# Optimization experiments

Measured on AMD Instinct MI355X. Metric: run time of the kernel, lower is better.

## Reference

```python
import jax, jax.numpy as jnp
import numpy as np

EMBED = 768
HEAD = 64
SEQ = 4096
BATCH = 4


def setup_inputs() -> dict:
    key = jax.random.key(0)
    ks = jax.random.split(key, 7)
    s = 1.0 / np.sqrt(EMBED)
    x = jax.random.normal(ks[0], (BATCH, SEQ, EMBED), dtype=jnp.float32)
    Wq = jax.random.uniform(ks[1], (EMBED, HEAD), jnp.float32, -s, s)
    bq = jax.random.uniform(ks[2], (HEAD,), jnp.float32, -s, s)
    Wk = jax.random.uniform(ks[3], (EMBED, HEAD), jnp.float32, -s, s)
    bk = jax.random.uniform(ks[4], (HEAD,), jnp.float32, -s, s)
    Wv = jax.random.uniform(ks[5], (EMBED, HEAD), jnp.float32, -s, s)
    bv = jax.random.uniform(ks[6], (HEAD,), jnp.float32, -s, s)
    return {"x": x, "Wq": Wq, "bq": bq, "Wk": Wk, "bk": bk, "Wv": Wv, "bv": bv}


def reference(x, Wq, bq, Wk, bk, Wv, bv):
    # x: [B,T,E]
    Q = x @ Wq + bq  # [B,T,H]
    K = x @ Wk + bk
    V = x @ Wv + bv
    scale = 1.0 / jnp.sqrt(jnp.asarray(HEAD, dtype=x.dtype))
    wei = jnp.einsum('bqh,bkh->bqk', Q, K) * scale  # [B,T,T]
    T = x.shape[1]
    causal = jnp.tril(jnp.ones((T, T), dtype=bool))
    wei = jnp.where(causal, wei, -jnp.inf)
    wei = jax.nn.softmax(wei, axis=-1)
    return jnp.einsum('bqk,bkh->bqh', wei, V)  # [B,T,H]
```

## Files before the change

### kernel.cpp

```cpp
#include <hip/hip_runtime.h>


#define BB 4
#define TT 4096
#define EE 768
#define HH 64
#define BT (BB*TT)

typedef __attribute__((ext_vector_type(8))) short short8;
typedef __attribute__((ext_vector_type(4))) float f32x4;
#define MFMA16(a,b,c) __builtin_amdgcn_mfma_f32_16x16x32_bf16(a,b,c,0,0,0)
#define QSCALE 0.18033688011112042f

static __device__ __forceinline__ float bflo(unsigned a){ return __uint_as_float(a << 16); }
static __device__ __forceinline__ unsigned short f2bf(float f){
    unsigned x = __float_as_uint(f);
    x += 0x7fffu + ((x >> 16) & 1u);
    return (unsigned short)(x >> 16);
}
template<int FP32>
static __device__ __forceinline__ float ldin(const void* p, int idx){
    if (FP32) return ((const float*)p)[idx];
    return bflo(((const unsigned short*)p)[idx]);
}

template<int FP32>
static __device__ void wt_body(const void* W, int wi, int e0, unsigned short* wt){
    __shared__ unsigned short ts[64 * 72];
    const int tid = threadIdx.x;
    #pragma unroll
    for (int p = 0; p < 2; p++){
        int i = p * 256 + tid;
        int r = i >> 3, g = i & 7;
        unsigned short v[8];
        if (FP32){
            const float* src = (const float*)W + (size_t)(e0 + r) * HH + g * 8;
            const float4 a = *(const float4*)src, b = *(const float4*)(src + 4);
            v[0]=f2bf(a.x); v[1]=f2bf(a.y); v[2]=f2bf(a.z); v[3]=f2bf(a.w);
            v[4]=f2bf(b.x); v[5]=f2bf(b.y); v[6]=f2bf(b.z); v[7]=f2bf(b.w);
        } else {
            const unsigned short* src = (const unsigned short*)W + (size_t)(e0 + r) * HH + g * 8;
            #pragma unroll
            for (int j = 0; j < 8; j++) v[j] = src[j];
        }
        #pragma unroll
        for (int j = 0; j < 8; j++) ts[r * 72 + g * 8 + j] = v[j];
    }
    __syncthreads();
    #pragma unroll
    for (int p = 0; p < 2; p++){
        int i = p * 256 + tid;
        int h = i >> 3, g = i & 7;
        unsigned short v[8];
        #pragma unroll
        for (int j = 0; j < 8; j++) v[j] = ts[(g * 8 + j) * 72 + h];
        unsigned short* dst = wt + (size_t)(wi * 64 + h) * EE + e0 + g * 8;
        uint4 pk;
        pk.x = (unsigned)v[0] | ((unsigned)v[1] << 16);
        pk.y = (unsigned)v[2] | ((unsigned)v[3] << 16);
        pk.z = (unsigned)v[4] | ((unsigned)v[5] << 16);
        pk.w = (unsigned)v[6] | ((unsigned)v[7] << 16);
        *(uint4*)dst = pk;
    }
}
__global__ __launch_bounds__(256) void wt_kernel(
    const unsigned short* xu, const void* Wq, const void* Wk, const void* Wv,
    unsigned short* wt, int* flag){
    __shared__ int cnt;
    const int tid = threadIdx.x;
    if (tid == 0) cnt = 0;
    __syncthreads();
    int c = 0;
    #pragma unroll
    for (int i = 0; i < 16; i++){
        unsigned u = xu[tid * 16 + i];
        unsigned e = (u >> 7) & 0xFFu;
        if (e >= 140u) c++;
    }
    atomicAdd(&cnt, c);
    __syncthreads();
    const int fp32 = (cnt > 32) ? 1 : 0;
    if (blockIdx.x == 0 && tid == 0) *flag = fp32;
    const int wi = blockIdx.x / 12;
    const int e0 = (blockIdx.x % 12) * 64;
    const void* W = (wi == 0) ? Wq : (wi == 1) ? Wk : Wv;
    if (fp32) wt_body<1>(W, wi, e0, wt);
    else      wt_body<0>(W, wi, e0, wt);
}

template<int FP32>
static __device__ void qkv_body(const void* x, const unsigned short* wt,
    const void* bq, const void* bk, const void* bv,
    unsigned short* Qw, unsigned short* Kw, unsigned short* VTw,
    unsigned short* xs, unsigned short* wsl)
{
    const int tid = threadIdx.x, lane = tid & 63, w = tid >> 6;
    const int l15 = lane & 15, quad = lane >> 4;
    const int z = blockIdx.x;
    const int m0 = (z >> 1) * 32;
    const int nh = z & 1;
    const int rh = (w & 1) * 16;
    const int ngl = (w >> 1) * 3;

    f32x4 acc[3];
    #pragma unroll
    for (int i = 0; i < 3; i++) acc[i] = (f32x4)(0.f);

    const int srow = tid >> 3, sg = tid & 7;

    for (int c = 0; c < 12; c++){
        const int c0 = c * 64;
        __syncthreads();
        {
            short8 v;
            if (FP32){
                const float* src = (const float*)x + (size_t)(m0 + srow) * EE + c0 + sg * 8;
                const float4 a = *(const float4*)src, b2 = *(const float4*)(src + 4);
                v[0]=(short)f2bf(a.x); v[1]=(short)f2bf(a.y); v[2]=(short)f2bf(a.z); v[3]=(short)f2bf(a.w);
                v[4]=(short)f2bf(b2.x); v[5]=(short)f2bf(b2.y); v[6]=(short)f2bf(b2.z); v[7]=(short)f2bf(b2.w);
            } else {
                v = *(const short8*)((const unsigned short*)x + (size_t)(m0 + srow) * EE + c0 + sg * 8);
            }
            *(short8*)&xs[srow * 72 + sg * 8] = v;
        }
        #pragma unroll
        for (int p = 0; p < 3; p++){
            int i = p * 256 + tid;
            int n = i >> 3, g2 = i & 7;
            *(short8*)&wsl[n * 72 + g2 * 8] =
                *(const short8*)(wt + (size_t)(nh * 96 + n) * EE + c0 + g2 * 8);
        }
        __syncthreads();
        #pragma unroll
        for (int kst = 0; kst < 2; kst++){
            const short8 a = *(const short8*)&xs[(rh + l15) * 72 + kst * 32 + quad * 8];
            #pragma unroll
            for (int nf = 0; nf < 3; nf++){
                const short8 bfr = *(const short8*)&wsl[((ngl + nf) * 16 + l15) * 72 + kst * 32 + quad * 8];
                acc[nf] = MFMA16(a, bfr, acc[nf]);
            }
        }
    }
    #pragma unroll
    for (int nf = 0; nf < 3; nf++){
        const int gi = nh * 6 + ngl + nf;
        const int wi = gi >> 2;
        const int h = (gi & 3) * 16 + l15;
        const void* bp = (wi == 0) ? bq : (wi == 1) ? bk : bv;
        const float bias = ldin<FP32>(bp, h);
        if (wi == 0){
            #pragma unroll
            for (int rr = 0; rr < 4; rr++){
                const int tok = m0 + rh + quad * 4 + rr;
                Qw[(size_t)tok * HH + h] = f2bf((acc[nf][rr] + bias) * QSCALE);
            }
        } else if (wi == 1){
            #pragma unroll
            for (int rr = 0; rr < 4; rr++){
                const int tok = m0 + rh + quad * 4 + rr;
                Kw[(size_t)tok * HH + h] = f2bf(acc[nf][rr] + bias);
            }
        } else {
            const int tok0 = m0 + rh + quad * 4;
            const int bloc = tok0 >> 12;
            const int tl = tok0 & 4095;
            uint2 pk;
            pk.x = (unsigned)f2bf(acc[nf][0] + bias) | ((unsigned)f2bf(acc[nf][1] + bias) << 16);
            pk.y = (unsigned)f2bf(acc[nf][2] + bias) | ((unsigned)f2bf(acc[nf][3] + bias) << 16);
            *(uint2*)&VTw[(size_t)(bloc * 64 + h) * TT + tl] = pk;
        }
    }
}
__global__ __launch_bounds__(256, 4) void qkv_kernel(
    const void* x, const unsigned short* wt,
    const void* bq, const void* bk, const void* bv,
    unsigned short* Qw, unsigned short* Kw, unsigned short* VTw, const int* flag){
    __shared__ unsigned short xs[32 * 72];
    __shared__ unsigned short wsl[96 * 72];
    if (*flag) qkv_body<1>(x, wt, bq, bk, bv, Qw, Kw, VTw, xs, wsl);
    else       qkv_body<0>(x, wt, bq, bk, bv, Qw, Kw, VTw, xs, wsl);
}

__global__ __launch_bounds__(512, 2) void attn_kernel(
    const unsigned short* __restrict__ Q,
    const unsigned short* __restrict__ K, const unsigned short* __restrict__ VT,
    void* __restrict__ out, const int* __restrict__ flag)
{
    __shared__ unsigned short sbuf[8][2304];
    __shared__ float lpart[8][32];

    const int mode = *flag;
    const int z = blockIdx.x;
    const int half = z >> 8;
    const int i0 = z & 255;
    const int b = i0 & 3;
    const int qt = half ? (i0 >> 2) : (127 - (i0 >> 2));
    const int q0 = qt * 32;
    const int nkb = (qt >> 1) + 1;
    const int tid = threadIdx.x;
    const int lane = tid & 63;
    const int w = tid >> 6;
    const int l15 = lane & 15, quad = lane >> 4;
    const int brow = b * TT;

    f32x4 O[2][4];
    float lsum[2][4];
    #pragma unroll
    for (int mt = 0; mt < 2; mt++)
        #pragma unroll
        for (int i = 0; i < 4; i++){ O[mt][i] = (f32x4)(0.f); lsum[mt][i] = 0.f; }

    if (w < nkb){
        short8 qf[2][2];
        #pragma unroll
        for (int mt = 0; mt < 2; mt++)
            #pragma unroll
            for (int kst = 0; kst < 2; kst++)
                qf[mt][kst] = *(const short8*)(Q + (size_t)(brow + q0 + mt * 16 + l15) * HH + kst * 32 + quad * 8);

        short8 kf[4][2];
        #pragma unroll
        for (int c = 0; c < 4; c++)
            #pragma unroll
            for (int kst = 0; kst < 2; kst++)
                kf[c][kst] = *(const short8*)(K + (size_t)(brow + w * 64 + c * 16 + l15) * HH + kst * 32 + quad * 8);

        for (int u = w; u < nkb; u += 8){
            const int k0 = u * 64;
            f32x4 sacc[2][4];
            #pragma unroll
            for (int mt = 0; mt < 2; mt++)
                #pragma unroll
                for (int c = 0; c < 4; c++){
                    sacc[mt][c] = (f32x4)(0.f);
                    sacc[mt][c] = MFMA16(qf[mt][0], kf[c][0], sacc[mt][c]);
                    sacc[mt][c] = MFMA16(qf[mt][1], kf[c][1], sacc[mt][c]);
                }
            short8 vf[4][2];
            #pragma unroll
            for (int c = 0; c < 4; c++)
                #pragma unroll
                for (int kst = 0; kst < 2; kst++)
                    vf[c][kst] = *(const short8*)(VT + (size_t)(b * 64 + c * 16 + l15) * TT + k0 + kst * 32 + quad * 8);
            if (u + 8 < nkb){
                const int kn0 = (u + 8) * 64;
                #pragma unroll
                for (int c = 0; c < 4; c++)
                    #pragma unroll
                    for (int kst = 0; kst < 2; kst++)
                        kf[c][kst] = *(const short8*)(K + (size_t)(brow + kn0 + c * 16 + l15) * HH + kst * 32 + quad * 8);
            }
            const bool diag = (u == nkb - 1);
            #pragma unroll
            for (int mt = 0; mt < 2; mt++){
                #pragma unroll
                for (int c = 0; c < 4; c++){
                    #pragma unroll
                    for (int rr = 0; rr < 4; rr++){
                        float sv = sacc[mt][c][rr];
                        if (diag){
                            const int kg = k0 + c * 16 + l15;
                            const int qg = q0 + mt * 16 + quad * 4 + rr;
                            sv = (kg <= qg) ? sv : -1e30f;
                        }
                        const float p = exp2f(sv);
                        lsum[mt][rr] += p;
                        sbuf[w][mt * 1152 + (quad * 4 + rr) * 72 + c * 16 + l15] = f2bf(p);
                    }
                }
            }
            #pragma unroll
            for (int mt = 0; mt < 2; mt++){
                const short8 pf0 = *(const short8*)&sbuf[w][mt * 1152 + l15 * 72 + quad * 8];
                const short8 pf1 = *(const short8*)&sbuf[w][mt * 1152 + l15 * 72 + 32 + quad * 8];
                #pragma unroll
                for (int c2 = 0; c2 < 4; c2++){
                    O[mt][c2] = MFMA16(pf0, vf[c2][0], O[mt][c2]);
                    O[mt][c2] = MFMA16(pf1, vf[c2][1], O[mt][c2]);
                }
            }
        }
        #pragma unroll
        for (int mt = 0; mt < 2; mt++)
            #pragma unroll
            for (int rr = 0; rr < 4; rr++){
                #pragma unroll
                for (int off = 1; off < 16; off <<= 1)
                    lsum[mt][rr] += __shfl_xor(lsum[mt][rr], off, 64);
            }
    }
    #pragma unroll
    for (int mt = 0; mt < 2; mt++)
        #pragma unroll
        for (int rr = 0; rr < 4; rr++){
            const int row = mt * 16 + quad * 4 + rr;
            #pragma unroll
            for (int c2 = 0; c2 < 4; c2++)
                sbuf[w][row * 72 + c2 * 16 + l15] = f2bf(O[mt][c2][rr]);
            if (l15 == 0) lpart[w][row] = lsum[mt][rr];
        }
    __syncthreads();
    #pragma unroll
    for (int i = 0; i < 4; i++){
        const int e = i * 512 + tid;
        const int r = e >> 6, h = e & 63;
        float num = 0.f, den = 0.f;
        #pragma unroll
        for (int ww = 0; ww < 8; ww++){
            num += bflo(sbuf[ww][r * 72 + h]);
            den += lpart[ww][r];
        }
        const float ov = num / den;
        const size_t gi = (size_t)(brow + q0 + r) * HH + h;
        if (mode) ((float*)out)[gi] = ov;
        else      ((unsigned short*)out)[gi] = f2bf(ov);
    }
}

extern "C" void kernel_launch(void* const* d_in, const int* in_sizes, int n_in,
                              void* d_out, int out_size, void* d_ws, size_t ws_size,
                              hipStream_t stream) {
    const void* x  = d_in[0];
    const void* Wq = d_in[1];
    const void* bq = d_in[2];
    const void* Wk = d_in[3];
    const void* bk = d_in[4];
    const void* Wv = d_in[5];
    const void* bv = d_in[6];

    unsigned short* Qw  = (unsigned short*)d_ws;
    unsigned short* Kw  = Qw + (size_t)BT * HH;
    unsigned short* VTw = Kw + (size_t)BT * HH;
    unsigned short* wt  = VTw + (size_t)BT * HH;
    int* flag  = (int*)(wt + (size_t)192 * EE);

    wt_kernel<<<36, 256, 0, stream>>>((const unsigned short*)x, Wq, Wk, Wv, wt, flag);
    qkv_kernel<<<1024, 256, 0, stream>>>(x, wt, bq, bk, bv, Qw, Kw, VTw, flag);
    attn_kernel<<<512, 512, 0, stream>>>(Qw, Kw, VTw, d_out, flag);
}
```

Before: 167.4 us.

## Split causal attention KV range across two blocks and add combine kernel

Each query tile's key/value range is now split into two halves handled by separate blocks, doubling the attention grid. Each block writes unnormalized partial numerators and denominators to workspace. A new combine kernel sums the two halves, normalizes, and writes the output in fp32 or bf16. This is meant to shorten the critical path of the longest causal tiles and balance work across CUs, at the cost of extra fp32 partial traffic to global memory and one more kernel launch.

```diff
diff --git a/kernel.cpp b/kernel.cpp
--- a/kernel.cpp
+++ b/kernel.cpp
@@ -184,19 +184,22 @@
 __global__ __launch_bounds__(512, 2) void attn_kernel(
     const unsigned short* __restrict__ Q,
     const unsigned short* __restrict__ K, const unsigned short* __restrict__ VT,
-    void* __restrict__ out, const int* __restrict__ flag)
+    float* __restrict__ pnum, float* __restrict__ pden)
 {
     __shared__ unsigned short sbuf[8][2304];
     __shared__ float lpart[8][32];
 
-    const int mode = *flag;
     const int z = blockIdx.x;
-    const int half = z >> 8;
-    const int i0 = z & 255;
+    const int half = z >> 9;
+    const int i0 = z & 511;
     const int b = i0 & 3;
-    const int qt = half ? (i0 >> 2) : (127 - (i0 >> 2));
+    const int qt = 127 - (i0 >> 2);
     const int q0 = qt * 32;
     const int nkb = (qt >> 1) + 1;
+    const int hk = (nkb + 1) >> 1;
+    const int u0 = half ? hk : 0;
+    const int u1 = half ? nkb : hk;
+    const int cnt = u1 - u0;
     const int tid = threadIdx.x;
     const int lane = tid & 63;
     const int w = tid >> 6;
@@ -210,7 +213,7 @@
         #pragma unroll
         for (int i = 0; i < 4; i++){ O[mt][i] = (f32x4)(0.f); lsum[mt][i] = 0.f; }
 
-    if (w < nkb){
+    if (w < cnt){
         short8 qf[2][2];
         #pragma unroll
         for (int mt = 0; mt < 2; mt++)
@@ -223,9 +226,9 @@
         for (int c = 0; c < 4; c++)
             #pragma unroll
             for (int kst = 0; kst < 2; kst++)
-                kf[c][kst] = *(const short8*)(K + (size_t)(brow + w * 64 + c * 16 + l15) * HH + kst * 32 + quad * 8);
-
-        for (int u = w; u < nkb; u += 8){
+                kf[c][kst] = *(const short8*)(K + (size_t)(brow + (u0 + w) * 64 + c * 16 + l15) * HH + kst * 32 + quad * 8);
+
+        for (int u = u0 + w; u < u1; u += 8){
             const int k0 = u * 64;
             f32x4 sacc[2][4];
             #pragma unroll
@@ -242,7 +245,7 @@
                 #pragma unroll
                 for (int kst = 0; kst < 2; kst++)
                     vf[c][kst] = *(const short8*)(VT + (size_t)(b * 64 + c * 16 + l15) * TT + k0 + kst * 32 + quad * 8);
-            if (u + 8 < nkb){
+            if (u + 8 < u1){
                 const int kn0 = (u + 8) * 64;
                 #pragma unroll
                 for (int c = 0; c < 4; c++)
@@ -300,6 +303,7 @@
             if (l15 == 0) lpart[w][row] = lsum[mt][rr];
         }
     __syncthreads();
+    const size_t pbase = ((size_t)half * 512 + i0) * 2048;
     #pragma unroll
     for (int i = 0; i < 4; i++){
         const int e = i * 512 + tid;
@@ -310,10 +314,50 @@
             num += bflo(sbuf[ww][r * 72 + h]);
             den += lpart[ww][r];
         }
-        const float ov = num / den;
-        const size_t gi = (size_t)(brow + q0 + r) * HH + h;
-        if (mode) ((float*)out)[gi] = ov;
-        else      ((unsigned short*)out)[gi] = f2bf(ov);
+        pnum[pbase + e] = num;
+        if (h == 0) pden[((size_t)half * 512 + i0) * 32 + r] = den;
+    }
+}
+
+__global__ __launch_bounds__(256) void combine_kernel(
+    const float* __restrict__ pnum, const float* __restrict__ pden,
+    void* __restrict__ out, const int* __restrict__ flag)
+{
+    const int mode = *flag;
+    const int g = blockIdx.x * 256 + threadIdx.x;
+    const int e0 = g * 8;
+    const int pidx = e0 >> 11;
+    const int o = e0 & 2047;
+    const int r = o >> 6, h = o & 63;
+    const int qt = 127 - (pidx >> 2);
+    const int b = pidx & 3;
+    const size_t base = (size_t)pidx * 2048 + o;
+    const float4 n0a = *(const float4*)&pnum[base];
+    const float4 n0b = *(const float4*)&pnum[base + 4];
+    const float4 n1a = *(const float4*)&pnum[(size_t)512 * 2048 + base];
+    const float4 n1b = *(const float4*)&pnum[(size_t)512 * 2048 + base + 4];
+    const float den = pden[pidx * 32 + r] + pden[512 * 32 + pidx * 32 + r];
+    const float inv = 1.f / den;
+    float ov[8] = {
+        (n0a.x + n1a.x) * inv, (n0a.y + n1a.y) * inv,
+        (n0a.z + n1a.z) * inv, (n0a.w + n1a.w) * inv,
+        (n0b.x + n1b.x) * inv, (n0b.y + n1b.y) * inv,
+        (n0b.z + n1b.z) * inv, (n0b.w + n1b.w) * inv };
+    const size_t gi = (size_t)(b * TT + qt * 32 + r) * HH + h;
+    if (mode){
+        float* op = (float*)out + gi;
+        float4 s0 = {ov[0], ov[1], ov[2], ov[3]};
+        float4 s1 = {ov[4], ov[5], ov[6], ov[7]};
+        *(float4*)op = s0;
+        *(float4*)(op + 4) = s1;
+    } else {
+        unsigned short* op = (unsigned short*)out + gi;
+        uint4 pk;
+        pk.x = (unsigned)f2bf(ov[0]) | ((unsigned)f2bf(ov[1]) << 16);
+        pk.y = (unsigned)f2bf(ov[2]) | ((unsigned)f2bf(ov[3]) << 16);
+        pk.z = (unsigned)f2bf(ov[4]) | ((unsigned)f2bf(ov[5]) << 16);
+        pk.w = (unsigned)f2bf(ov[6]) | ((unsigned)f2bf(ov[7]) << 16);
+        *(uint4*)op = pk;
     }
 }
 
@@ -333,8 +377,11 @@
     unsigned short* VTw = Kw + (size_t)BT * HH;
     unsigned short* wt  = VTw + (size_t)BT * HH;
     int* flag  = (int*)(wt + (size_t)192 * EE);
+    float* pnum = (float*)(flag + 4);
+    float* pden = pnum + (size_t)2 * 512 * 2048;
 
     wt_kernel<<<36, 256, 0, stream>>>((const unsigned short*)x, Wq, Wk, Wv, wt, flag);
     qkv_kernel<<<1024, 256, 0, stream>>>(x, wt, bq, bk, bv, Qw, Kw, VTw, flag);
-    attn_kernel<<<512, 512, 0, stream>>>(Qw, Kw, VTw, d_out, flag);
-}
+    attn_kernel<<<1024, 512, 0, stream>>>(Qw, Kw, VTw, pnum, pden);
+    combine_kernel<<<512, 256, 0, stream>>>(pnum, pden, d_out, flag);
+}
```

New measurement: 171.7 us. 1.03x slower.
